# Performance work log

Measured on AMD Instinct MI355X. Metric: run time of the kernel, lower is better.

## Reference

```python
import jax, jax.numpy as jnp
import numpy as np

N = 50000      # nodes
E = 1_600_000  # edges
IN, HID, OUT, NC = 384, 128, 64, 2
EPS = 1e-5


def layer_norm(x, g, b):
    mu = x.mean(-1, keepdims=True)
    v = ((x - mu) ** 2).mean(-1, keepdims=True)
    return (x - mu) / jnp.sqrt(v + EPS) * g + b


def gat_conv(x, src, dst, ea, W, a_s, a_d, We, a_e, bias, n):
    """PyG GATConv, heads=1, edge_dim=1, add_self_loops with fill_value='mean'."""
    h = x @ W  # [n, F]
    # self-loop edge_attr = mean of incoming edge_attr per destination node
    ones = jnp.ones((src.shape[0],), h.dtype)
    cnt = jax.ops.segment_sum(ones, dst, num_segments=n)
    esum = jax.ops.segment_sum(ea, dst, num_segments=n)
    loop_ea = esum / jnp.maximum(cnt, 1.0)[:, None]
    loop = jnp.arange(n)
    s2 = jnp.concatenate([src, loop])
    d2 = jnp.concatenate([dst, loop])
    ea2 = jnp.concatenate([ea, loop_ea], axis=0)
    al_s = h @ a_s          # [n]
    al_d = h @ a_d          # [n]
    al_e = (ea2 @ We) @ a_e  # [E+n]
    logits = jax.nn.leaky_relu(al_s[s2] + al_d[d2] + al_e, 0.2)
    m = jax.ops.segment_max(logits, d2, num_segments=n)  # every node has a self loop
    ex = jnp.exp(logits - m[d2])
    den = jax.ops.segment_sum(ex, d2, num_segments=n)
    alpha = ex / den[d2]
    out = jax.ops.segment_sum(alpha[:, None] * h[s2], d2, num_segments=n)
    return out + bias


def setup_inputs() -> dict:
    key = jax.random.key(0)
    ks = jax.random.split(key, 20)
    def xav(k, fan_in, fan_out):
        s = float(np.sqrt(6.0 / (fan_in + fan_out)))
        return jax.random.uniform(k, (fan_in, fan_out), jnp.float32, -s, s)
    x = jax.random.normal(ks[0], (N, IN), jnp.float32)
    edge_index = jax.random.randint(ks[1], (2, E), 0, N)
    edge_attr = jax.random.normal(ks[2], (E, 1), jnp.float32)
    return {
        "x": x, "edge_index": edge_index, "edge_attr": edge_attr,
        "ln1_g": jnp.ones((IN,), jnp.float32), "ln1_b": jnp.zeros((IN,), jnp.float32),
        "fc1_w": xav(ks[3], IN, HID), "fc1_b": jnp.zeros((HID,), jnp.float32),
        "conv1_w": xav(ks[4], HID, HID),
        "conv1_as": jax.random.normal(ks[5], (HID,), jnp.float32) * 0.1,
        "conv1_ad": jax.random.normal(ks[6], (HID,), jnp.float32) * 0.1,
        "conv1_we": xav(ks[7], 1, HID),
        "conv1_ae": jax.random.normal(ks[8], (HID,), jnp.float32) * 0.1,
        "conv1_b": jnp.zeros((HID,), jnp.float32),
        "conv2_w": xav(ks[9], HID, OUT),
        "conv2_as": jax.random.normal(ks[10], (OUT,), jnp.float32) * 0.1,
        "conv2_ad": jax.random.normal(ks[11], (OUT,), jnp.float32) * 0.1,
        "conv2_we": xav(ks[12], 1, OUT),
        "conv2_ae": jax.random.normal(ks[13], (OUT,), jnp.float32) * 0.1,
        "conv2_b": jnp.zeros((OUT,), jnp.float32),
        "ln2_g": jnp.ones((OUT,), jnp.float32), "ln2_b": jnp.zeros((OUT,), jnp.float32),
        "fc2_w": xav(ks[14], OUT, NC), "fc2_b": jnp.zeros((NC,), jnp.float32),
    }


def reference(x, edge_index, edge_attr,
              ln1_g, ln1_b, fc1_w, fc1_b,
              conv1_w, conv1_as, conv1_ad, conv1_we, conv1_ae, conv1_b,
              conv2_w, conv2_as, conv2_ad, conv2_we, conv2_ae, conv2_b,
              ln2_g, ln2_b, fc2_w, fc2_b):
    src, dst = edge_index[0], edge_index[1]
    n = x.shape[0]
    h = layer_norm(x, ln1_g, ln1_b) @ fc1_w + fc1_b
    h = gat_conv(h, src, dst, edge_attr, conv1_w, conv1_as, conv1_ad, conv1_we, conv1_ae, conv1_b, n)
    h = jax.nn.leaky_relu(h, 0.01)
    h = gat_conv(h, src, dst, edge_attr, conv2_w, conv2_as, conv2_ad, conv2_we, conv2_ae, conv2_b, n)
    h = jax.nn.leaky_relu(h, 0.01)
    out = layer_norm(h, ln2_g, ln2_b) @ fc2_w + fc2_b
    return out
```

## Files before the change

kernel.cpp:

```cpp
#include <hip/hip_runtime.h>

#define NN 50000
#define NE 1600000
#define CAP 64
#define NBIN 196
#define NBLK 391
#define RUNCAP 48
#define FC1B 782

typedef __attribute__((ext_vector_type(8))) short short8v;
typedef __attribute__((ext_vector_type(4))) float f32x4;

__device__ __forceinline__ float wsum(float v) {
#pragma unroll
  for (int m = 32; m > 0; m >>= 1) v += __shfl_xor(v, m, 64);
  return v;
}
__device__ __forceinline__ float wmax(float v) {
#pragma unroll
  for (int m = 32; m > 0; m >>= 1) v = fmaxf(v, __shfl_xor(v, m, 64));
  return v;
}
__device__ __forceinline__ float leakyf(float x, float s) { return x > 0.f ? x : s * x; }

__device__ __forceinline__ unsigned short bfr(float f) {
  unsigned u = __float_as_uint(f);
  return (unsigned short)((u + 0x7FFFu + ((u >> 16) & 1u)) >> 16);
}
__device__ __forceinline__ unsigned pack2(float a, float b) {
  return (unsigned)bfr(a) | ((unsigned)bfr(b) << 16);
}
__device__ __forceinline__ float bflo(unsigned u) { return __uint_as_float(u << 16); }
__device__ __forceinline__ float bfhi(unsigned u) { return __uint_as_float(u & 0xFFFF0000u); }

__global__ __launch_bounds__(256) void k_pre1(
    const int* __restrict__ src, const int* __restrict__ dst, const float* __restrict__ ea,
    int2* __restrict__ binRun, int* __restrict__ runLen,
    const float* __restrict__ fc1w, const float* __restrict__ g, const float* __restrict__ b,
    const float* __restrict__ fb, const float* __restrict__ we1, const float* __restrict__ ae1,
    const float* __restrict__ we2, const float* __restrict__ ae2,
    const float* __restrict__ cw1, const float* __restrict__ cw2,
    unsigned short* __restrict__ WgF, unsigned short* __restrict__ W1F,
    unsigned short* __restrict__ W2F, float* __restrict__ u, float* __restrict__ v,
    float* __restrict__ ce) {
  __shared__ int cur[NBIN];
  __shared__ float r1[128], r2[128];
  int tid = threadIdx.x, bid = blockIdx.x;
  if (bid < NBLK) {
    for (int i = tid; i < NBIN; i += 256) cur[i] = 0;
    __syncthreads();
    int2* myRun = binRun + (size_t)bid * NBIN * RUNCAP;
    int base4 = bid * 1024;
#pragma unroll
    for (int i = 0; i < 4; ++i) {
      int t4 = base4 + i * 256 + tid;
      if (t4 < NE / 4) {
        int4 s = ((const int4*)src)[t4];
        int4 d = ((const int4*)dst)[t4];
        float4 a = ((const float4*)ea)[t4];
        int bin, p;
        bin = d.x >> 8; p = atomicAdd(&cur[bin], 1);
        if (p < RUNCAP) myRun[bin * RUNCAP + p] = make_int2(s.x | ((d.x & 255) << 16), __float_as_int(a.x));
        bin = d.y >> 8; p = atomicAdd(&cur[bin], 1);
        if (p < RUNCAP) myRun[bin * RUNCAP + p] = make_int2(s.y | ((d.y & 255) << 16), __float_as_int(a.y));
        bin = d.z >> 8; p = atomicAdd(&cur[bin], 1);
        if (p < RUNCAP) myRun[bin * RUNCAP + p] = make_int2(s.z | ((d.z & 255) << 16), __float_as_int(a.z));
        bin = d.w >> 8; p = atomicAdd(&cur[bin], 1);
        if (p < RUNCAP) myRun[bin * RUNCAP + p] = make_int2(s.w | ((d.w & 255) << 16), __float_as_int(a.w));
      }
    }
    __syncthreads();
    for (int i = tid; i < NBIN; i += 256) runLen[bid * NBIN + i] = min(cur[i], RUNCAP);
  } else if (bid < NBLK + 64) {
    int vb = bid - NBLK;
    int t0 = vb * 256 + tid;
    const int stride = 64 * 256;
    for (int i = t0; i < 8 * 12 * 512; i += stride) {
      int j = i & 7, lane = (i >> 3) & 63, tk = i >> 9;
      int ks = tk % 12, t = tk / 12;
      int c = t * 16 + (lane & 15);
      int k = ks * 32 + (lane >> 4) * 8 + j;
      WgF[i] = bfr(g[k] * fc1w[k * 128 + c]);
    }
    for (int i = t0; i < 8 * 4 * 512; i += stride) {
      int j = i & 7, lane = (i >> 3) & 63, tk = i >> 9;
      int ks = tk & 3, t = tk >> 2;
      int c = t * 16 + (lane & 15);
      int k = ks * 32 + (lane >> 4) * 8 + j;
      W1F[i] = bfr(cw1[k * 128 + c]);
    }
    for (int i = t0; i < 4 * 4 * 512; i += stride) {
      int j = i & 7, lane = (i >> 3) & 63, tk = i >> 9;
      int ks = tk & 3, t = tk >> 2;
      int c = t * 16 + (lane & 15);
      int k = ks * 32 + (lane >> 4) * 8 + j;
      W2F[i] = bfr(cw2[k * 64 + c]);
    }
  } else {
    int c = tid;
    if (c < 128) {
      float ua = 0.f, va = 0.f;
#pragma unroll 4
      for (int k = 0; k < 384; ++k) {
        float w = fc1w[k * 128 + c];
        ua += g[k] * w;
        va += b[k] * w;
      }
      u[c] = ua;
      v[c] = va + fb[c];
      r1[c] = we1[c] * ae1[c];
      r2[c] = (c < 64) ? we2[c] * ae2[c] : 0.f;
    }
    __syncthreads();
    for (int o = 64; o > 0; o >>= 1) {
      if (c < o) { r1[c] += r1[c + o]; r2[c] += r2[c + o]; }
      __syncthreads();
    }
    if (c == 0) { ce[0] = r1[0]; ce[1] = r2[0]; }
  }
}

__global__ __launch_bounds__(256) void k_main1(
    const float* __restrict__ x, const unsigned short* __restrict__ WgF,
    const unsigned short* __restrict__ W1F, const float* __restrict__ u,
    const float* __restrict__ v, const float* __restrict__ a_s,
    const float* __restrict__ a_d, unsigned short* __restrict__ Hb,
    float* __restrict__ al_s, float* __restrict__ al_d,
    const int2* __restrict__ binRun, const int* __restrict__ runLen,
    int2* __restrict__ edat, int* __restrict__ cnt) {
  __shared__ __align__(16) unsigned short xs[64][392];
  __shared__ float mu_s[64], rs_s[64];
  int tid = threadIdx.x, bid = blockIdx.x;
  if (bid < NBIN) {
    int j = bid;
    int* cur = (int*)&xs[0][0];
    int* rl = cur + 256;
    cur[tid] = 0;
    for (int i = tid; i < NBLK; i += 256) rl[i] = runLen[i * NBIN + j];
    __syncthreads();
    const int TOT = NBLK * RUNCAP;
    for (int g = tid; g < TOT; g += 256) {
      int b = g / RUNCAP, r = g - b * RUNCAP;
      if (r < rl[b]) {
        int2 rec = binRun[(size_t)b * NBIN * RUNCAP + j * RUNCAP + r];
        int srcv = rec.x & 0xFFFF;
        int dlow = rec.x >> 16;
        int dstv = (j << 8) | dlow;
        int p = atomicAdd(&cur[dlow], 1);
        if (p < CAP) edat[(size_t)dstv * CAP + p] = make_int2(srcv, rec.y);
      }
    }
    __syncthreads();
    int dstv = (j << 8) | tid;
    if (dstv < NN) cnt[dstv] = min(cur[tid], CAP);
    return;
  }
  int fb1 = bid - NBIN;
  int wv = tid >> 6, lane = tid & 63;
  int lrow = lane & 15, lk = lane >> 4;
  long n0 = (long)fb1 * 64;
  for (int rr = 0; rr < 16; ++rr) {
    int r = wv * 16 + rr;
    long gr = n0 + r;
    if (gr > NN - 1) gr = NN - 1;
    const float* xr = x + gr * 384;
#pragma unroll
    for (int js = 0; js < 3; ++js) {
      float2 val = *(const float2*)&xr[lane * 2 + 128 * js];
      *(unsigned*)&xs[r][lane * 2 + 128 * js] = pack2(val.x, val.y);
    }
  }
  __syncthreads();
  const unsigned short* abase = &xs[wv * 16 + lrow][lk * 8];
  union { short8v v8; unsigned short us[8]; } ONE;
#pragma unroll
  for (int j = 0; j < 8; ++j) ONE.us[j] = 0x3F80;
  f32x4 acc[8] = {};
  f32x4 accS = {0.f, 0.f, 0.f, 0.f}, accQ = {0.f, 0.f, 0.f, 0.f};
  for (int ks = 0; ks < 12; ++ks) {
    short8v A = *(const short8v*)(abase + ks * 32);
    accS = __builtin_amdgcn_mfma_f32_16x16x32_bf16(A, ONE.v8, accS, 0, 0, 0);
    accQ = __builtin_amdgcn_mfma_f32_16x16x32_bf16(A, A, accQ, 0, 0, 0);
#pragma unroll
    for (int t = 0; t < 8; ++t) {
      short8v B = *(const short8v*)&WgF[((t * 12 + ks) * 64 + lane) * 8];
      acc[t] = __builtin_amdgcn_mfma_f32_16x16x32_bf16(A, B, acc[t], 0, 0, 0);
    }
  }
  {
    int dr = lrow - lk * 4;
    if (dr >= 0 && dr < 4) {
      float sum = accS[dr];
      float sq = accQ[dr];
      float mu = sum * (1.f / 384.f);
      float var = sq * (1.f / 384.f) - mu * mu;
      mu_s[wv * 16 + lrow] = mu;
      rs_s[wv * 16 + lrow] = rsqrtf(fmaxf(var, 0.f) + 1e-5f);
    }
  }
  float uc[8], vc[8];
#pragma unroll
  for (int t = 0; t < 8; ++t) {
    int c = t * 16 + lrow;
    uc[t] = u[c];
    vc[t] = v[c];
  }
#pragma unroll
  for (int reg = 0; reg < 4; ++reg) {
    int rl2 = wv * 16 + lk * 4 + reg;
    float mu = mu_s[rl2], rs = rs_s[rl2];
#pragma unroll
    for (int t = 0; t < 8; ++t) {
      float val = rs * (acc[t][reg] - mu * uc[t]) + vc[t];
      xs[rl2][t * 16 + lrow] = bfr(val);
    }
  }
  __syncthreads();
  f32x4 acc2[8] = {};
#pragma unroll
  for (int ks = 0; ks < 4; ++ks) {
    short8v A = *(const short8v*)(abase + ks * 32);
#pragma unroll
    for (int t = 0; t < 8; ++t) {
      short8v B = *(const short8v*)&W1F[((t * 4 + ks) * 64 + lane) * 8];
      acc2[t] = __builtin_amdgcn_mfma_f32_16x16x32_bf16(A, B, acc2[t], 0, 0, 0);
    }
  }
  float asv[8], adv[8];
#pragma unroll
  for (int t = 0; t < 8; ++t) {
    asv[t] = a_s[t * 16 + lrow];
    adv[t] = a_d[t * 16 + lrow];
  }
#pragma unroll
  for (int reg = 0; reg < 4; ++reg) {
    float ps = 0.f, pd = 0.f;
#pragma unroll
    for (int t = 0; t < 8; ++t) {
      ps += acc2[t][reg] * asv[t];
      pd += acc2[t][reg] * adv[t];
    }
#pragma unroll
    for (int m = 1; m < 16; m <<= 1) {
      ps += __shfl_xor(ps, m, 64);
      pd += __shfl_xor(pd, m, 64);
    }
    long rg = n0 + wv * 16 + lk * 4 + reg;
    if (rg < NN) {
      if (lrow == 0) { al_s[rg] = ps; al_d[rg] = pd; }
#pragma unroll
      for (int t = 0; t < 8; ++t) Hb[rg * 128 + t * 16 + lrow] = bfr(acc2[t][reg]);
    }
  }
}

template <int NT>
__global__ __launch_bounds__(256) void k_mxw(
    const unsigned short* __restrict__ Xb, const unsigned short* __restrict__ WF,
    const float* __restrict__ a_s, const float* __restrict__ a_d,
    unsigned short* __restrict__ Hb, float* __restrict__ al_s, float* __restrict__ al_d) {
  __shared__ __align__(16) unsigned short xs[64][136];
  int tid = threadIdx.x, wv = tid >> 6, lane = tid & 63;
  int lrow = lane & 15, lk = lane >> 4;
  long n0 = (long)blockIdx.x * 64;
  for (int rr = 0; rr < 16; ++rr) {
    int r = wv * 16 + rr;
    long gr = n0 + r;
    if (gr > NN - 1) gr = NN - 1;
    *(unsigned*)&xs[r][lane * 2] = *(const unsigned*)&Xb[gr * 128 + lane * 2];
  }
  __syncthreads();
  const unsigned short* abase = &xs[wv * 16 + lrow][lk * 8];
  f32x4 acc[NT] = {};
#pragma unroll
  for (int ks = 0; ks < 4; ++ks) {
    short8v A = *(const short8v*)(abase + ks * 32);
#pragma unroll
    for (int t = 0; t < NT; ++t) {
      short8v B = *(const short8v*)&WF[((t * 4 + ks) * 64 + lane) * 8];
      acc[t] = __builtin_amdgcn_mfma_f32_16x16x32_bf16(A, B, acc[t], 0, 0, 0);
    }
  }
  float asv[NT], adv[NT];
#pragma unroll
  for (int t = 0; t < NT; ++t) {
    asv[t] = a_s[t * 16 + lrow];
    adv[t] = a_d[t * 16 + lrow];
  }
#pragma unroll
  for (int reg = 0; reg < 4; ++reg) {
    float ps = 0.f, pd = 0.f;
#pragma unroll
    for (int t = 0; t < NT; ++t) {
      ps += acc[t][reg] * asv[t];
      pd += acc[t][reg] * adv[t];
    }
#pragma unroll
    for (int m = 1; m < 16; m <<= 1) {
      ps += __shfl_xor(ps, m, 64);
      pd += __shfl_xor(pd, m, 64);
    }
    long rg = n0 + wv * 16 + lk * 4 + reg;
    if (rg < NN) {
      if (lrow == 0) { al_s[rg] = ps; al_d[rg] = pd; }
#pragma unroll
      for (int t = 0; t < NT; ++t) Hb[rg * (NT * 16) + t * 16 + lrow] = bfr(acc[t][reg]);
    }
  }
}

template <int F, bool OB, bool FUSE_LN>
__global__ __launch_bounds__(256) void k_agg(
    const unsigned short* __restrict__ Hb, const float* __restrict__ al_s,
    const float* __restrict__ al_d, const float* __restrict__ cep,
    const int* __restrict__ cntA, const int2* __restrict__ edat,
    const float* __restrict__ bias, void* __restrict__ outp,
    const float* __restrict__ g2, const float* __restrict__ b2,
    const float* __restrict__ w2, const float* __restrict__ fb2) {
  int wv = threadIdx.x >> 6, lane = threadIdx.x & 63;
  int i = blockIdx.x * 4 + wv;
  int cnt = min(cntA[i], CAP);
  float ce = *cep;
  float ald = al_d[i];
  bool valid = lane < cnt;
  int s = 0;
  float eav = 0.f, lg = -1e30f;
  if (valid) {
    int2 ed = edat[(size_t)i * CAP + lane];
    s = ed.x;
    eav = __int_as_float(ed.y);
    lg = leakyf(al_s[s] + ald + ce * eav, 0.2f);
  }
  float easum = wsum(eav);
  float loop_ea = easum / fmaxf((float)cnt, 1.f);
  float lg_self = leakyf(al_s[i] + ald + ce * loop_ea, 0.2f);
  float mx = fmaxf(wmax(lg), lg_self);
  float e = valid ? __expf(lg - mx) : 0.f;
  float es_ = __expf(lg_self - mx);
  float den = wsum(e) + es_;
  float acc0, acc1 = 0.f;
  if (F == 128) {
    unsigned u = *(const unsigned*)&Hb[(size_t)i * 128 + 2 * lane];
    acc0 = es_ * bflo(u);
    acc1 = es_ * bfhi(u);
  } else {
    acc0 = es_ * __uint_as_float(((unsigned)Hb[(size_t)i * 64 + lane]) << 16);
  }
  int t = 0;
  for (; t + 8 <= cnt; t += 8) {
    float et[8];
    unsigned uu[8];
#pragma unroll
    for (int j = 0; j < 8; ++j) {
      et[j] = __shfl(e, t + j, 64);
      int sj = __shfl(s, t + j, 64);
      if (F == 128)
        uu[j] = *(const unsigned*)&Hb[(size_t)sj * 128 + 2 * lane];
      else
        uu[j] = ((unsigned)Hb[(size_t)sj * 64 + lane]) << 16;
    }
#pragma unroll
    for (int j = 0; j < 8; ++j) {
      if (F == 128) {
        acc0 += et[j] * bflo(uu[j]);
        acc1 += et[j] * bfhi(uu[j]);
      } else {
        acc0 += et[j] * __uint_as_float(uu[j]);
      }
    }
  }
  for (; t < cnt; ++t) {
    float et = __shfl(e, t, 64);
    int st = __shfl(s, t, 64);
    if (F == 128) {
      unsigned u = *(const unsigned*)&Hb[(size_t)st * 128 + 2 * lane];
      acc0 += et * bflo(u);
      acc1 += et * bfhi(u);
    } else {
      acc0 += et * __uint_as_float(((unsigned)Hb[(size_t)st * 64 + lane]) << 16);
    }
  }
  float inv = 1.f / den;
  if (F == 128) {
    float2 bv = *(const float2*)&bias[2 * lane];
    float o0 = leakyf(acc0 * inv + bv.x, 0.01f);
    float o1 = leakyf(acc1 * inv + bv.y, 0.01f);
    if (OB) {
      ((unsigned*)outp)[(size_t)i * 64 + lane] = pack2(o0, o1);
    } else {
      *(float2*)&((float*)outp)[(size_t)i * 128 + 2 * lane] = make_float2(o0, o1);
    }
  } else {
    float o = leakyf(acc0 * inv + bias[lane], 0.01f);
    if (FUSE_LN) {
      float sum = wsum(o);
      float ssum = wsum(o * o);
      float mu = sum * (1.f / 64.f);
      float var = ssum * (1.f / 64.f) - mu * mu;
      float rs = rsqrtf(var + 1e-5f);
      float xn = (o - mu) * rs * g2[lane] + b2[lane];
      float q0 = wsum(xn * w2[lane * 2 + 0]);
      float q1 = wsum(xn * w2[lane * 2 + 1]);
      if (lane == 0) {
        ((float*)outp)[(size_t)i * 2 + 0] = q0 + fb2[0];
        ((float*)outp)[(size_t)i * 2 + 1] = q1 + fb2[1];
      }
    } else {
      ((float*)outp)[(size_t)i * 64 + lane] = o;
    }
  }
}

extern "C" void kernel_launch(void* const* d_in, const int* in_sizes, int n_in,
                              void* d_out, int out_size, void* d_ws, size_t ws_size,
                              hipStream_t stream) {
  const int N = NN;
  const float* x = (const float*)d_in[0];
  const int* ei = (const int*)d_in[1];
  const float* ea = (const float*)d_in[2];
  const float* ln1_g = (const float*)d_in[3];
  const float* ln1_b = (const float*)d_in[4];
  const float* fc1_w = (const float*)d_in[5];
  const float* fc1_b = (const float*)d_in[6];
  const float* c1_w = (const float*)d_in[7];
  const float* c1_as = (const float*)d_in[8];
  const float* c1_ad = (const float*)d_in[9];
  const float* c1_we = (const float*)d_in[10];
  const float* c1_ae = (const float*)d_in[11];
  const float* c1_b = (const float*)d_in[12];
  const float* c2_w = (const float*)d_in[13];
  const float* c2_as = (const float*)d_in[14];
  const float* c2_ad = (const float*)d_in[15];
  const float* c2_we = (const float*)d_in[16];
  const float* c2_ae = (const float*)d_in[17];
  const float* c2_b = (const float*)d_in[18];
  const float* ln2_g = (const float*)d_in[19];
  const float* ln2_b = (const float*)d_in[20];
  const float* fc2_w = (const float*)d_in[21];
  const float* fc2_b = (const float*)d_in[22];

  const int* src = ei;
  const int* dst = ei + NE;

  unsigned short* spare = (unsigned short*)d_ws;
  unsigned short* Hb = spare + (size_t)N * 128;
  unsigned short* o1b = Hb + (size_t)N * 128;
  float* al_s = (float*)(o1b + (size_t)N * 128);
  float* al_d = al_s + N;
  float* cebuf = al_d + N;
  float* uvec = cebuf + 4;
  float* vvec = uvec + 128;
  unsigned short* WgF = (unsigned short*)(vvec + 128);
  unsigned short* W1F = WgF + 8 * 12 * 512;
  unsigned short* W2F = W1F + 8 * 4 * 512;
  int* cnt = (int*)(W2F + 4 * 4 * 512);
  int* runLen = cnt + N;
  int2* edat = (int2*)((((uintptr_t)(runLen + NBLK * NBIN)) + 15) & ~(uintptr_t)15);
  int2* binRun = (int2*)(edat + (size_t)N * CAP);

  size_t need = ((char*)(binRun + (size_t)NBLK * NBIN * RUNCAP)) - (char*)d_ws;
  if (ws_size < need) return;

  k_pre1<<<NBLK + 64 + 1, 256, 0, stream>>>(src, dst, ea, binRun, runLen,
                                            fc1_w, ln1_g, ln1_b, fc1_b,
                                            c1_we, c1_ae, c2_we, c2_ae, c1_w, c2_w,
                                            WgF, W1F, W2F, uvec, vvec, cebuf);
  k_main1<<<NBIN + FC1B, 256, 0, stream>>>(x, WgF, W1F, uvec, vvec, c1_as, c1_ad,
                                           Hb, al_s, al_d, binRun, runLen, edat, cnt);

  k_agg<128, true, false><<<N / 4, 256, 0, stream>>>(Hb, al_s, al_d, cebuf + 0, cnt, edat,
                                                     c1_b, o1b, nullptr, nullptr, nullptr,
                                                     nullptr);
  k_mxw<4><<<FC1B, 256, 0, stream>>>(o1b, W2F, c2_as, c2_ad, Hb, al_s, al_d);
  k_agg<64, false, true><<<N / 4, 256, 0, stream>>>(Hb, al_s, al_d, cebuf + 1, cnt, edat,
                                                    c2_b, d_out, ln2_g, ln2_b, fc2_w, fc2_b);
}
```

Before: 204.1 us.

## Split each node's edge aggregation across two wavefronts with shared-memory reduction

The aggregation kernel now gives each destination node a 128-thread block, with two wavefronts that each handle half of the incoming edges. Edge-attribute sums, max logits, softmax denominators and partial accumulators are combined through shared memory and two block barriers. The goal is to halve the serial gather loop per wavefront and expose more memory-level parallelism on the random Hb row gathers. In exchange it adds block syncs, LDS traffic, more blocks to schedule, and the self-loop term is computed redundantly in both waves.

```diff
diff --git a/kernel.cpp b/kernel.cpp
--- a/kernel.cpp
+++ b/kernel.cpp
@@ -310,44 +310,60 @@
 }
 
 template <int F, bool OB, bool FUSE_LN>
-__global__ __launch_bounds__(256) void k_agg(
+__global__ __launch_bounds__(128) void k_agg(
     const unsigned short* __restrict__ Hb, const float* __restrict__ al_s,
     const float* __restrict__ al_d, const float* __restrict__ cep,
     const int* __restrict__ cntA, const int2* __restrict__ edat,
     const float* __restrict__ bias, void* __restrict__ outp,
     const float* __restrict__ g2, const float* __restrict__ b2,
     const float* __restrict__ w2, const float* __restrict__ fb2) {
+  __shared__ float sh_ea[2], sh_mx[2], sh_den;
+  __shared__ float sh_acc[128];
   int wv = threadIdx.x >> 6, lane = threadIdx.x & 63;
-  int i = blockIdx.x * 4 + wv;
+  int i = blockIdx.x;
   int cnt = min(cntA[i], CAP);
   float ce = *cep;
   float ald = al_d[i];
-  bool valid = lane < cnt;
+  int c0 = (cnt + 1) >> 1;
+  int myc = wv ? (cnt >> 1) : c0;
+  int base = wv ? c0 : 0;
+  bool valid = lane < myc;
   int s = 0;
   float eav = 0.f, lg = -1e30f;
   if (valid) {
-    int2 ed = edat[(size_t)i * CAP + lane];
+    int2 ed = edat[(size_t)i * CAP + base + lane];
     s = ed.x;
     eav = __int_as_float(ed.y);
     lg = leakyf(al_s[s] + ald + ce * eav, 0.2f);
   }
-  float easum = wsum(eav);
+  float ea_p = wsum(eav);
+  float mx_p = wmax(lg);
+  if (lane == 0) {
+    sh_ea[wv] = ea_p;
+    sh_mx[wv] = mx_p;
+  }
+  __syncthreads();
+  float easum = sh_ea[0] + sh_ea[1];
+  float mxn = fmaxf(sh_mx[0], sh_mx[1]);
   float loop_ea = easum / fmaxf((float)cnt, 1.f);
   float lg_self = leakyf(al_s[i] + ald + ce * loop_ea, 0.2f);
-  float mx = fmaxf(wmax(lg), lg_self);
+  float mx = fmaxf(mxn, lg_self);
   float e = valid ? __expf(lg - mx) : 0.f;
   float es_ = __expf(lg_self - mx);
-  float den = wsum(e) + es_;
-  float acc0, acc1 = 0.f;
-  if (F == 128) {
-    unsigned u = *(const unsigned*)&Hb[(size_t)i * 128 + 2 * lane];
-    acc0 = es_ * bflo(u);
-    acc1 = es_ * bfhi(u);
-  } else {
-    acc0 = es_ * __uint_as_float(((unsigned)Hb[(size_t)i * 64 + lane]) << 16);
+  float den_p = wsum(e);
+  float acc0 = 0.f, acc1 = 0.f;
+  if (wv == 0) {
+    den_p += es_;
+    if (F == 128) {
+      unsigned u = *(const unsigned*)&Hb[(size_t)i * 128 + 2 * lane];
+      acc0 = es_ * bflo(u);
+      acc1 = es_ * bfhi(u);
+    } else {
+      acc0 = es_ * __uint_as_float(((unsigned)Hb[(size_t)i * 64 + lane]) << 16);
+    }
   }
   int t = 0;
-  for (; t + 8 <= cnt; t += 8) {
+  for (; t + 8 <= myc; t += 8) {
     float et[8];
     unsigned uu[8];
 #pragma unroll
@@ -369,7 +385,7 @@
       }
     }
   }
-  for (; t < cnt; ++t) {
+  for (; t < myc; ++t) {
     float et = __shfl(e, t, 64);
     int st = __shfl(s, t, 64);
     if (F == 128) {
@@ -380,33 +396,52 @@
       acc0 += et * __uint_as_float(((unsigned)Hb[(size_t)st * 64 + lane]) << 16);
     }
   }
-  float inv = 1.f / den;
-  if (F == 128) {
-    float2 bv = *(const float2*)&bias[2 * lane];
-    float o0 = leakyf(acc0 * inv + bv.x, 0.01f);
-    float o1 = leakyf(acc1 * inv + bv.y, 0.01f);
-    if (OB) {
-      ((unsigned*)outp)[(size_t)i * 64 + lane] = pack2(o0, o1);
+  if (wv == 1) {
+    if (F == 128) {
+      sh_acc[lane] = acc0;
+      sh_acc[64 + lane] = acc1;
     } else {
-      *(float2*)&((float*)outp)[(size_t)i * 128 + 2 * lane] = make_float2(o0, o1);
-    }
-  } else {
-    float o = leakyf(acc0 * inv + bias[lane], 0.01f);
-    if (FUSE_LN) {
-      float sum = wsum(o);
-      float ssum = wsum(o * o);
-      float mu = sum * (1.f / 64.f);
-      float var = ssum * (1.f / 64.f) - mu * mu;
-      float rs = rsqrtf(var + 1e-5f);
-      float xn = (o - mu) * rs * g2[lane] + b2[lane];
-      float q0 = wsum(xn * w2[lane * 2 + 0]);
-      float q1 = wsum(xn * w2[lane * 2 + 1]);
-      if (lane == 0) {
-        ((float*)outp)[(size_t)i * 2 + 0] = q0 + fb2[0];
-        ((float*)outp)[(size_t)i * 2 + 1] = q1 + fb2[1];
+      sh_acc[lane] = acc0;
+    }
+    if (lane == 0) sh_den = den_p;
+  }
+  __syncthreads();
+  if (wv == 0) {
+    float den = den_p + sh_den;
+    if (F == 128) {
+      acc0 += sh_acc[lane];
+      acc1 += sh_acc[64 + lane];
+    } else {
+      acc0 += sh_acc[lane];
+    }
+    float inv = 1.f / den;
+    if (F == 128) {
+      float2 bv = *(const float2*)&bias[2 * lane];
+      float o0 = leakyf(acc0 * inv + bv.x, 0.01f);
+      float o1 = leakyf(acc1 * inv + bv.y, 0.01f);
+      if (OB) {
+        ((unsigned*)outp)[(size_t)i * 64 + lane] = pack2(o0, o1);
+      } else {
+        *(float2*)&((float*)outp)[(size_t)i * 128 + 2 * lane] = make_float2(o0, o1);
       }
     } else {
-      ((float*)outp)[(size_t)i * 64 + lane] = o;
+      float o = leakyf(acc0 * inv + bias[lane], 0.01f);
+      if (FUSE_LN) {
+        float sum = wsum(o);
+        float ssum = wsum(o * o);
+        float mu = sum * (1.f / 64.f);
+        float var = ssum * (1.f / 64.f) - mu * mu;
+        float rs = rsqrtf(var + 1e-5f);
+        float xn = (o - mu) * rs * g2[lane] + b2[lane];
+        float q0 = wsum(xn * w2[lane * 2 + 0]);
+        float q1 = wsum(xn * w2[lane * 2 + 1]);
+        if (lane == 0) {
+          ((float*)outp)[(size_t)i * 2 + 0] = q0 + fb2[0];
+          ((float*)outp)[(size_t)i * 2 + 1] = q1 + fb2[1];
+        }
+      } else {
+        ((float*)outp)[(size_t)i * 64 + lane] = o;
+      }
     }
   }
 }
@@ -468,10 +503,10 @@
   k_main1<<<NBIN + FC1B, 256, 0, stream>>>(x, WgF, W1F, uvec, vvec, c1_as, c1_ad,
                                            Hb, al_s, al_d, binRun, runLen, edat, cnt);
 
-  k_agg<128, true, false><<<N / 4, 256, 0, stream>>>(Hb, al_s, al_d, cebuf + 0, cnt, edat,
-                                                     c1_b, o1b, nullptr, nullptr, nullptr,
-                                                     nullptr);
+  k_agg<128, true, false><<<N, 128, 0, stream>>>(Hb, al_s, al_d, cebuf + 0, cnt, edat,
+                                                 c1_b, o1b, nullptr, nullptr, nullptr,
+                                                 nullptr);
   k_mxw<4><<<FC1B, 256, 0, stream>>>(o1b, W2F, c2_as, c2_ad, Hb, al_s, al_d);
-  k_agg<64, false, true><<<N / 4, 256, 0, stream>>>(Hb, al_s, al_d, cebuf + 1, cnt, edat,
-                                                    c2_b, d_out, ln2_g, ln2_b, fc2_w, fc2_b);
-}
+  k_agg<64, false, true><<<N, 128, 0, stream>>>(Hb, al_s, al_d, cebuf + 1, cnt, edat,
+                                                c2_b, d_out, ln2_g, ln2_b, fc2_w, fc2_b);
+}
```

New measurement: 239.0 us. 17.1% more time.
